# Performance work log

Measured on AMD Instinct MI355X. Metric: run time of the kernel, lower is better.

The kernel has to match this reference:

```python
import jax, jax.numpy as jnp
import numpy as np

N_NODES = 10000
N_EDGES = 640000
IN_DIM = 128
OUT_DIM = 128


def setup_inputs() -> dict:
    key = jax.random.key(0)
    k1, k2, k3, k4, k5 = jax.random.split(key, 5)
    h = jax.random.normal(k1, (N_NODES, IN_DIM), dtype=jnp.float32)
    src = jax.random.randint(k2, (N_EDGES,), 0, N_NODES, dtype=jnp.int32)
    dst = jax.random.randint(k3, (N_EDGES,), 0, N_NODES, dtype=jnp.int32)
    # nn.Linear default init: U(-1/sqrt(fan_in), 1/sqrt(fan_in)); scale normals similarly
    W_fc = jax.random.normal(k4, (OUT_DIM, IN_DIM), dtype=jnp.float32) / np.sqrt(IN_DIM)
    W_attn = jax.random.normal(k5, (1, 2 * OUT_DIM), dtype=jnp.float32) / np.sqrt(2 * OUT_DIM)
    return {"h": h, "src": src, "dst": dst, "W_fc": W_fc, "W_attn": W_attn}


def reference(h, src, dst, W_fc, W_attn):
    n = h.shape[0]
    # z = fc(h)
    z = h @ W_fc.T                                   # [N, out]
    # edge attention: attn_fc(cat([z_src, z_dst])) == z_src @ a_s + z_dst @ a_d
    a_src = W_attn[0, :OUT_DIM]                      # [out]
    a_dst = W_attn[0, OUT_DIM:]                      # [out]
    e = z @ a_src                                    # [N] per-node src contribution
    f = z @ a_dst                                    # [N] per-node dst contribution
    score = e[src] + f[dst]                          # [E] edge logits
    # segment softmax over incoming edges of each dst node
    m = jax.ops.segment_max(score, dst, num_segments=n)   # [N]
    m = jnp.where(jnp.isfinite(m), m, 0.0)                # guard empty segments
    ex = jnp.exp(score - m[dst])                           # [E]
    den = jax.ops.segment_sum(ex, dst, num_segments=n)     # [N]
    alpha = ex / jnp.where(den > 0, den, 1.0)[dst]          # [E]
    # weighted scatter-sum of source z into dst
    msg = alpha[:, None] * z[src]                           # [E, out]
    h_out = jax.ops.segment_sum(msg, dst, num_segments=n)  # [N, out]
    return h_out
```

## Files before the change

### kernel.cpp

```cpp
#include <hip/hip_runtime.h>

#define NN 10000
#define NE 640000
#define DIM 128
#define SB 64
#define SEPB (NE / SB)
#define FCN 32
#define FCB ((NN + FCN - 1) / FCN)
#define DCAP 128

static __device__ __forceinline__ unsigned short f2bf(float f) {
    unsigned u = __float_as_uint(f);
    unsigned r = (u + 0x7FFFu + ((u >> 16) & 1u)) >> 16;
    return (unsigned short)r;
}
static __device__ __forceinline__ float bfhi(unsigned u) { return __uint_as_float(u & 0xFFFF0000u); }
static __device__ __forceinline__ float bflo(unsigned u) { return __uint_as_float(u << 16); }

__global__ __launch_bounds__(512, 2) void scatfc_kernel(
    const int* __restrict__ src, const int* __restrict__ dst,
    unsigned short* __restrict__ blkoffs,
    unsigned short* __restrict__ esrc16,
    const float* __restrict__ h, const float* __restrict__ W,
    const float* __restrict__ Wa, unsigned short* __restrict__ zb,
    float* __restrict__ e)
{
    __shared__ int smem[10256];
    const int bid = blockIdx.x, t = threadIdx.x;

    if (bid < SB) {
        int* cnt = smem;
        int* wsum = smem + 10240;
        int4* c4 = (int4*)cnt;
        for (int i = t; i < NN / 4; i += 512) c4[i] = make_int4(0, 0, 0, 0);
        __syncthreads();

        const int4* d4 = (const int4*)(dst + bid * SEPB);
        const int4* s4 = (const int4*)(src + bid * SEPB);
        for (int i = t; i < SEPB / 4; i += 512) {
            int4 d = d4[i];
            atomicAdd(&cnt[d.x], 1); atomicAdd(&cnt[d.y], 1);
            atomicAdd(&cnt[d.z], 1); atomicAdd(&cnt[d.w], 1);
        }
        __syncthreads();

        constexpr int C = 20;
        const int lane = t & 63, wid = t >> 6;
        int loc[C];
        int base = t * C, s = 0;
        #pragma unroll
        for (int j = 0; j < C; ++j) {
            int idx = base + j;
            int v = (idx < NN) ? cnt[idx] : 0;
            loc[j] = s; s += v;
        }
        int x = s;
        #pragma unroll
        for (int o = 1; o <= 32; o <<= 1) {
            int y = __shfl_up(x, o, 64);
            if (lane >= o) x += y;
        }
        if (lane == 63) wsum[wid] = x;
        __syncthreads();
        if (t == 0) {
            int run = 0;
            #pragma unroll
            for (int i2 = 0; i2 < 8; ++i2) { int tmp = wsum[i2]; wsum[i2] = run; run += tmp; }
        }
        __syncthreads();
        const int texcl = wsum[wid] + (x - s);
        #pragma unroll
        for (int j = 0; j < C; ++j) {
            int idx = base + j;
            if (idx < NN) cnt[idx] = texcl + loc[j];
        }
        __syncthreads();

        unsigned short* bo = blkoffs + (size_t)bid * (NN + 1);
        for (int v = t; v < NN; v += 512) bo[v] = (unsigned short)cnt[v];
        if (t == 0) bo[NN] = (unsigned short)SEPB;
        __syncthreads();

        unsigned short* eo = esrc16 + (size_t)bid * SEPB;
        for (int i = t; i < SEPB / 4; i += 512) {
            int4 d = d4[i]; int4 sv = s4[i];
            int r;
            r = atomicAdd(&cnt[d.x], 1); eo[r] = (unsigned short)sv.x;
            r = atomicAdd(&cnt[d.y], 1); eo[r] = (unsigned short)sv.y;
            r = atomicAdd(&cnt[d.z], 1); eo[r] = (unsigned short)sv.z;
            r = atomicAdd(&cnt[d.w], 1); eo[r] = (unsigned short)sv.w;
        }
    } else {
        float* hs = (float*)smem;
        float* wt = hs + FCN * DIM;
        const int jl = t & 31, jq = jl * 4;
        const int ng = t >> 5;
        const int i0 = (bid - SB) * FCN;

        const float4* h4 = (const float4*)h;
        float4* hs4 = (float4*)hs;
        #pragma unroll
        for (int p = 0; p < 2; ++p) {
            int u = t + p * 512;
            int gi = i0 + (u >> 5);
            hs4[u] = (gi < NN) ? h4[(size_t)gi * 32 + (u & 31)]
                               : make_float4(0.f, 0.f, 0.f, 0.f);
        }

        const float4* W4 = (const float4*)W;
        float acc[2][4] = {};
        for (int kt = 0; kt < 4; ++kt) {
            __syncthreads();
            #pragma unroll
            for (int p = 0; p < 2; ++p) {
                int idx = t + p * 512;
                int row = idx >> 3, q4 = idx & 7;
                float4 wv = W4[(size_t)row * 32 + kt * 8 + q4];
                wt[(q4 * 4 + 0) * 132 + row] = wv.x;
                wt[(q4 * 4 + 1) * 132 + row] = wv.y;
                wt[(q4 * 4 + 2) * 132 + row] = wv.z;
                wt[(q4 * 4 + 3) * 132 + row] = wv.w;
            }
            __syncthreads();
            #pragma unroll
            for (int kk4 = 0; kk4 < 8; ++kk4) {
                float4 wj0 = *(const float4*)&wt[(kk4 * 4 + 0) * 132 + jq];
                float4 wj1 = *(const float4*)&wt[(kk4 * 4 + 1) * 132 + jq];
                float4 wj2 = *(const float4*)&wt[(kk4 * 4 + 2) * 132 + jq];
                float4 wj3 = *(const float4*)&wt[(kk4 * 4 + 3) * 132 + jq];
                #pragma unroll
                for (int m = 0; m < 2; ++m) {
                    float4 hv = *(const float4*)&hs[(2 * ng + m) * DIM + kt * 32 + kk4 * 4];
                    acc[m][0] += hv.x * wj0.x + hv.y * wj1.x + hv.z * wj2.x + hv.w * wj3.x;
                    acc[m][1] += hv.x * wj0.y + hv.y * wj1.y + hv.z * wj2.y + hv.w * wj3.y;
                    acc[m][2] += hv.x * wj0.z + hv.y * wj1.z + hv.z * wj2.z + hv.w * wj3.z;
                    acc[m][3] += hv.x * wj0.w + hv.y * wj1.w + hv.z * wj2.w + hv.w * wj3.w;
                }
            }
        }

        const float a0 = Wa[jq], a1 = Wa[jq + 1], a2 = Wa[jq + 2], a3 = Wa[jq + 3];
        #pragma unroll
        for (int m = 0; m < 2; ++m) {
            int gi = i0 + 2 * ng + m;
            float ep = acc[m][0] * a0 + acc[m][1] * a1 + acc[m][2] * a2 + acc[m][3] * a3;
            #pragma unroll
            for (int o = 16; o > 0; o >>= 1) ep += __shfl_xor(ep, o, 64);
            if (gi < NN) {
                ushort4 zo;
                zo.x = f2bf(acc[m][0]); zo.y = f2bf(acc[m][1]);
                zo.z = f2bf(acc[m][2]); zo.w = f2bf(acc[m][3]);
                *(ushort4*)&zb[(size_t)gi * DIM + jq] = zo;
                if (jl == 0) e[gi] = ep;
            }
        }
    }
}

__global__ __launch_bounds__(256) void agg_kernel(
    const unsigned short* __restrict__ blkoffs, const unsigned short* __restrict__ esrc16,
    const float* __restrict__ e, const unsigned* __restrict__ zb32,
    float* __restrict__ out)
{
    __shared__ int   es[4][DCAP];
    __shared__ float ew[4][DCAP];
    const int w = threadIdx.x >> 6, lane = threadIdx.x & 63;
    const int v = blockIdx.x * 4 + w;
    int* esw = es[w];
    float* eww = ew[w];

    const unsigned short* bo = blkoffs + (size_t)lane * (NN + 1) + v;
    const int start = bo[0];
    const int cell  = bo[1] - start;

    int x = cell;
    #pragma unroll
    for (int o = 1; o <= 32; o <<= 1) {
        int y = __shfl_up(x, o, 64);
        if (lane >= o) x += y;
    }
    int deg = __shfl(x, 63, 64);
    if (deg > DCAP) deg = DCAP;
    int base = x - cell;

    const unsigned short* ep = esrc16 + (size_t)lane * SEPB + start;
    for (int j = 0; j < cell; ++j) {
        int tgt = base + j;
        if (tgt < DCAP) {
            int s = ep[j];
            esw[tgt] = s;
            eww[tgt] = e[s];
        }
    }

    float lm = -3.4e38f;
    for (int i = lane; i < deg; i += 64) lm = fmaxf(lm, eww[i]);
    #pragma unroll
    for (int o = 32; o > 0; o >>= 1) lm = fmaxf(lm, __shfl_xor(lm, o, 64));

    float ls = 0.f;
    for (int i = lane; i < deg; i += 64) {
        float p = __expf(eww[i] - lm);
        eww[i] = p; ls += p;
    }
    #pragma unroll
    for (int o = 32; o > 0; o >>= 1) ls += __shfl_xor(ls, o, 64);
    const float inv = (ls > 0.f) ? (1.f / ls) : 0.f;

    const uint2* zb2 = (const uint2*)zb32;
    const int half = lane >> 5, hl = lane & 31;
    float a0 = 0.f, a1 = 0.f, a2 = 0.f, a3 = 0.f;
    int i = half;
    for (; i + 6 < deg; i += 8) {
        int   t0 = esw[i],  t1 = esw[i + 2],  t2 = esw[i + 4],  t3 = esw[i + 6];
        float w0 = eww[i],  w1 = eww[i + 2],  w2 = eww[i + 4],  w3 = eww[i + 6];
        uint2 u0 = zb2[(size_t)t0 * 32 + hl];
        uint2 u1 = zb2[(size_t)t1 * 32 + hl];
        uint2 u2 = zb2[(size_t)t2 * 32 + hl];
        uint2 u3 = zb2[(size_t)t3 * 32 + hl];
        a0 += w0 * bflo(u0.x); a1 += w0 * bfhi(u0.x);
        a2 += w0 * bflo(u0.y); a3 += w0 * bfhi(u0.y);
        a0 += w1 * bflo(u1.x); a1 += w1 * bfhi(u1.x);
        a2 += w1 * bflo(u1.y); a3 += w1 * bfhi(u1.y);
        a0 += w2 * bflo(u2.x); a1 += w2 * bfhi(u2.x);
        a2 += w2 * bflo(u2.y); a3 += w2 * bfhi(u2.y);
        a0 += w3 * bflo(u3.x); a1 += w3 * bfhi(u3.x);
        a2 += w3 * bflo(u3.y); a3 += w3 * bfhi(u3.y);
    }
    for (; i < deg; i += 2) {
        int s = esw[i]; float p = eww[i];
        uint2 u = zb2[(size_t)s * 32 + hl];
        a0 += p * bflo(u.x); a1 += p * bfhi(u.x);
        a2 += p * bflo(u.y); a3 += p * bfhi(u.y);
    }
    a0 += __shfl_xor(a0, 32, 64);
    a1 += __shfl_xor(a1, 32, 64);
    a2 += __shfl_xor(a2, 32, 64);
    a3 += __shfl_xor(a3, 32, 64);
    if (half == 0) {
        float4 r;
        r.x = a0 * inv; r.y = a1 * inv; r.z = a2 * inv; r.w = a3 * inv;
        *(float4*)&out[(size_t)v * DIM + 4 * hl] = r;
    }
}

extern "C" void kernel_launch(void* const* d_in, const int* in_sizes, int n_in,
                              void* d_out, int out_size, void* d_ws, size_t ws_size,
                              hipStream_t stream)
{
    const float* h     = (const float*)d_in[0];
    const int*   src   = (const int*)d_in[1];
    const int*   dst   = (const int*)d_in[2];
    const float* Wfc   = (const float*)d_in[3];
    const float* Wattn = (const float*)d_in[4];
    float* out = (float*)d_out;

    unsigned short* zb      = (unsigned short*)d_ws;
    float*          e       = (float*)(zb + (size_t)NN * DIM);
    unsigned short* blkoffs = (unsigned short*)(e + 10016);
    unsigned short* esrc16  = blkoffs + (size_t)SB * (NN + 1) + 16;

    scatfc_kernel<<<SB + FCB, 512, 0, stream>>>(src, dst, blkoffs, esrc16,
                                                h, Wfc, Wattn, zb, e);
    agg_kernel<<<NN / 4, 256, 0, stream>>>(blkoffs, esrc16, e, (const unsigned*)zb, out);
}
```

Measured before the change: 45.97 us.

## Fold softmax exp into source features and pack per-block CSR offsets

```diff
diff --git a/kernel.cpp b/kernel.cpp
--- a/kernel.cpp
+++ b/kernel.cpp
@@ -8,6 +8,7 @@
 #define FCN 32
 #define FCB ((NN + FCN - 1) / FCN)
 #define DCAP 128
+#define ZSTRIDE 136
 
 static __device__ __forceinline__ unsigned short f2bf(float f) {
     unsigned u = __float_as_uint(f);
@@ -19,11 +20,10 @@
 
 __global__ __launch_bounds__(512, 2) void scatfc_kernel(
     const int* __restrict__ src, const int* __restrict__ dst,
-    unsigned short* __restrict__ blkoffs,
+    unsigned* __restrict__ bo32,
     unsigned short* __restrict__ esrc16,
     const float* __restrict__ h, const float* __restrict__ W,
-    const float* __restrict__ Wa, unsigned short* __restrict__ zb,
-    float* __restrict__ e)
+    const float* __restrict__ Wa, unsigned short* __restrict__ zbx)
 {
     __shared__ int smem[10256];
     const int bid = blockIdx.x, t = threadIdx.x;
@@ -76,9 +76,12 @@
         }
         __syncthreads();
 
-        unsigned short* bo = blkoffs + (size_t)bid * (NN + 1);
-        for (int v = t; v < NN; v += 512) bo[v] = (unsigned short)cnt[v];
-        if (t == 0) bo[NN] = (unsigned short)SEPB;
+        unsigned* bo = bo32 + (size_t)bid * NN;
+        for (int v = t; v < NN; v += 512) {
+            int st = cnt[v];
+            int nx = (v + 1 < NN) ? cnt[v + 1] : SEPB;
+            bo[v] = ((unsigned)st << 16) | (unsigned)(nx - st);
+        }
         __syncthreads();
 
         unsigned short* eo = esrc16 + (size_t)bid * SEPB;
@@ -147,31 +150,30 @@
             #pragma unroll
             for (int o = 16; o > 0; o >>= 1) ep += __shfl_xor(ep, o, 64);
             if (gi < NN) {
+                float u = __expf(ep);
                 ushort4 zo;
-                zo.x = f2bf(acc[m][0]); zo.y = f2bf(acc[m][1]);
-                zo.z = f2bf(acc[m][2]); zo.w = f2bf(acc[m][3]);
-                *(ushort4*)&zb[(size_t)gi * DIM + jq] = zo;
-                if (jl == 0) e[gi] = ep;
+                zo.x = f2bf(u * acc[m][0]); zo.y = f2bf(u * acc[m][1]);
+                zo.z = f2bf(u * acc[m][2]); zo.w = f2bf(u * acc[m][3]);
+                *(ushort4*)&zbx[(size_t)gi * ZSTRIDE + jq] = zo;
+                if (jl == 0)
+                    *(float*)(zbx + (size_t)gi * ZSTRIDE + 128) = u;
             }
         }
     }
 }
 
 __global__ __launch_bounds__(256) void agg_kernel(
-    const unsigned short* __restrict__ blkoffs, const unsigned short* __restrict__ esrc16,
-    const float* __restrict__ e, const unsigned* __restrict__ zb32,
-    float* __restrict__ out)
+    const unsigned* __restrict__ bo32, const unsigned short* __restrict__ esrc16,
+    const unsigned short* __restrict__ zbx, float* __restrict__ out)
 {
-    __shared__ int   es[4][DCAP];
-    __shared__ float ew[4][DCAP];
+    __shared__ int es[4][DCAP];
     const int w = threadIdx.x >> 6, lane = threadIdx.x & 63;
     const int v = blockIdx.x * 4 + w;
     int* esw = es[w];
-    float* eww = ew[w];
-
-    const unsigned short* bo = blkoffs + (size_t)lane * (NN + 1) + v;
-    const int start = bo[0];
-    const int cell  = bo[1] - start;
+
+    unsigned q = bo32[(size_t)lane * NN + v];
+    const int start = (int)(q >> 16);
+    const int cell  = (int)(q & 0xFFFFu);
 
     int x = cell;
     #pragma unroll
@@ -186,58 +188,43 @@
     const unsigned short* ep = esrc16 + (size_t)lane * SEPB + start;
     for (int j = 0; j < cell; ++j) {
         int tgt = base + j;
-        if (tgt < DCAP) {
-            int s = ep[j];
-            esw[tgt] = s;
-            eww[tgt] = e[s];
-        }
-    }
-
-    float lm = -3.4e38f;
-    for (int i = lane; i < deg; i += 64) lm = fmaxf(lm, eww[i]);
-    #pragma unroll
-    for (int o = 32; o > 0; o >>= 1) lm = fmaxf(lm, __shfl_xor(lm, o, 64));
-
-    float ls = 0.f;
-    for (int i = lane; i < deg; i += 64) {
-        float p = __expf(eww[i] - lm);
-        eww[i] = p; ls += p;
-    }
-    #pragma unroll
-    for (int o = 32; o > 0; o >>= 1) ls += __shfl_xor(ls, o, 64);
-    const float inv = (ls > 0.f) ? (1.f / ls) : 0.f;
-
-    const uint2* zb2 = (const uint2*)zb32;
+        if (tgt < DCAP) esw[tgt] = ep[j];
+    }
+
+    const uint2* zb2 = (const uint2*)zbx;
     const int half = lane >> 5, hl = lane & 31;
-    float a0 = 0.f, a1 = 0.f, a2 = 0.f, a3 = 0.f;
+    float a0 = 0.f, a1 = 0.f, a2 = 0.f, a3 = 0.f, den = 0.f;
     int i = half;
     for (; i + 6 < deg; i += 8) {
-        int   t0 = esw[i],  t1 = esw[i + 2],  t2 = esw[i + 4],  t3 = esw[i + 6];
-        float w0 = eww[i],  w1 = eww[i + 2],  w2 = eww[i + 4],  w3 = eww[i + 6];
-        uint2 u0 = zb2[(size_t)t0 * 32 + hl];
-        uint2 u1 = zb2[(size_t)t1 * 32 + hl];
-        uint2 u2 = zb2[(size_t)t2 * 32 + hl];
-        uint2 u3 = zb2[(size_t)t3 * 32 + hl];
-        a0 += w0 * bflo(u0.x); a1 += w0 * bfhi(u0.x);
-        a2 += w0 * bflo(u0.y); a3 += w0 * bfhi(u0.y);
-        a0 += w1 * bflo(u1.x); a1 += w1 * bfhi(u1.x);
-        a2 += w1 * bflo(u1.y); a3 += w1 * bfhi(u1.y);
-        a0 += w2 * bflo(u2.x); a1 += w2 * bfhi(u2.x);
-        a2 += w2 * bflo(u2.y); a3 += w2 * bfhi(u2.y);
-        a0 += w3 * bflo(u3.x); a1 += w3 * bfhi(u3.x);
-        a2 += w3 * bflo(u3.y); a3 += w3 * bfhi(u3.y);
+        int s0 = esw[i], s1 = esw[i + 2], s2 = esw[i + 4], s3 = esw[i + 6];
+        uint2 u0 = zb2[(size_t)s0 * 34 + hl];
+        uint2 u1 = zb2[(size_t)s1 * 34 + hl];
+        uint2 u2 = zb2[(size_t)s2 * 34 + hl];
+        uint2 u3 = zb2[(size_t)s3 * 34 + hl];
+        float w0 = *(const float*)(zbx + (size_t)s0 * ZSTRIDE + 128);
+        float w1 = *(const float*)(zbx + (size_t)s1 * ZSTRIDE + 128);
+        float w2 = *(const float*)(zbx + (size_t)s2 * ZSTRIDE + 128);
+        float w3 = *(const float*)(zbx + (size_t)s3 * ZSTRIDE + 128);
+        a0 += bflo(u0.x); a1 += bfhi(u0.x); a2 += bflo(u0.y); a3 += bfhi(u0.y);
+        a0 += bflo(u1.x); a1 += bfhi(u1.x); a2 += bflo(u1.y); a3 += bfhi(u1.y);
+        a0 += bflo(u2.x); a1 += bfhi(u2.x); a2 += bflo(u2.y); a3 += bfhi(u2.y);
+        a0 += bflo(u3.x); a1 += bfhi(u3.x); a2 += bflo(u3.y); a3 += bfhi(u3.y);
+        den += w0 + w1 + w2 + w3;
     }
     for (; i < deg; i += 2) {
-        int s = esw[i]; float p = eww[i];
-        uint2 u = zb2[(size_t)s * 32 + hl];
-        a0 += p * bflo(u.x); a1 += p * bfhi(u.x);
-        a2 += p * bflo(u.y); a3 += p * bfhi(u.y);
+        int s = esw[i];
+        uint2 u = zb2[(size_t)s * 34 + hl];
+        den += *(const float*)(zbx + (size_t)s * ZSTRIDE + 128);
+        a0 += bflo(u.x); a1 += bfhi(u.x);
+        a2 += bflo(u.y); a3 += bfhi(u.y);
     }
     a0 += __shfl_xor(a0, 32, 64);
     a1 += __shfl_xor(a1, 32, 64);
     a2 += __shfl_xor(a2, 32, 64);
     a3 += __shfl_xor(a3, 32, 64);
+    den += __shfl_xor(den, 32, 64);
     if (half == 0) {
+        const float inv = (den > 0.f) ? (1.f / den) : 0.f;
         float4 r;
         r.x = a0 * inv; r.y = a1 * inv; r.z = a2 * inv; r.w = a3 * inv;
         *(float4*)&out[(size_t)v * DIM + 4 * hl] = r;
@@ -255,12 +242,11 @@
     const float* Wattn = (const float*)d_in[4];
     float* out = (float*)d_out;
 
-    unsigned short* zb      = (unsigned short*)d_ws;
-    float*          e       = (float*)(zb + (size_t)NN * DIM);
-    unsigned short* blkoffs = (unsigned short*)(e + 10016);
-    unsigned short* esrc16  = blkoffs + (size_t)SB * (NN + 1) + 16;
-
-    scatfc_kernel<<<SB + FCB, 512, 0, stream>>>(src, dst, blkoffs, esrc16,
-                                                h, Wfc, Wattn, zb, e);
-    agg_kernel<<<NN / 4, 256, 0, stream>>>(blkoffs, esrc16, e, (const unsigned*)zb, out);
-}
+    unsigned short* zbx    = (unsigned short*)d_ws;
+    unsigned*       bo32   = (unsigned*)(zbx + (size_t)NN * ZSTRIDE);
+    unsigned short* esrc16 = (unsigned short*)(bo32 + (size_t)SB * NN);
+
+    scatfc_kernel<<<SB + FCB, 512, 0, stream>>>(src, dst, bo32, esrc16,
+                                                h, Wfc, Wattn, zbx);
+    agg_kernel<<<NN / 4, 256, 0, stream>>>(bo32, esrc16, zbx, out);
+}
```

Result: slower. 47.18 us (+2.6%).
